# Kernel optimization log

Measured on AMD Instinct MI355X. Metric: run time of the kernel, lower is better.

The kernel has to match this reference:

```python
import jax, jax.numpy as jnp
import numpy as np

C, H, W = 64, 282, 282
PILLAR_SIZE = 0.16
RANGE_MIN = -22.0


def _scatter_forward(PFN_input, PFN_output):
    # PFN_input: [B, 2, P, 1] pillar (x, y) coords; PFN_output: [B, C, P] features
    x = PFN_input[:, 0, :, 0]  # [B, P]
    y = PFN_input[:, 1, :, 0]  # [B, P]
    valid = x != 0  # original uses nonzero(PFN_input[b,0,:,0]) as pillar list
    # digitize into grid cells (equivalent of get_grid over arange(-22,22,0.16))
    xg = jnp.floor((x - RANGE_MIN) / PILLAR_SIZE).astype(jnp.int32)
    yg = jnp.floor((y - RANGE_MIN) / PILLAR_SIZE).astype(jnp.int32)
    # route invalid pillars to an out-of-bounds index; jax scatter drops OOB updates
    xg = jnp.where(valid, jnp.clip(xg, 0, W - 1), W)
    yg = jnp.where(valid, jnp.clip(yg, 0, H - 1), H)

    def scatter_one(xgb, ygb, feats):  # xgb,ygb: [P]; feats: [C, P]
        canvas = jnp.zeros((C, H, W), feats.dtype)
        return canvas.at[:, ygb, xgb].set(feats)

    return jax.vmap(scatter_one)(xg, yg, PFN_output)  # [B, C, H, W]


def setup_inputs() -> dict:
    key = jax.random.key(0)
    k1, k2 = jax.random.split(key)
    B, P = 4, 12000
    PFN_input = jax.random.uniform(k1, (B, 2, P, 1), dtype=jnp.float32,
                                   minval=-22.0, maxval=22.0)
    PFN_output = jax.random.normal(k2, (B, C, P), dtype=jnp.float32)
    return {"PFN_input": PFN_input, "PFN_output": PFN_output}


def reference(PFN_input, PFN_output):
    return _scatter_forward(PFN_input, PFN_output)
```

## Files before the change

### kernel.cpp

```cpp
#include <hip/hip_runtime.h>

#define NB 4
#define NC 64
#define NH 282
#define NW 282
#define NP 12000
#define HWC (NH * NW)
#define QHW (HWC / 4)
#define CLAIM_INTS (NB * HWC)
#define SPLIT 8

__device__ __align__(16) int g_claim[CLAIM_INTS];

__global__ void pps_init_kernel() {
    int gid = blockIdx.x * blockDim.x + threadIdx.x;
    if (gid < CLAIM_INTS / 4) {
        ((int4*)g_claim)[gid] = make_int4(-1, -1, -1, -1);
    }
}

__global__ void pps_claim_kernel(const float* __restrict__ pfn_in) {
    int gid = blockIdx.x * blockDim.x + threadIdx.x;
    if (gid >= NB * NP) return;
    int b = gid / NP;
    int p = gid - b * NP;
    const float* base = pfn_in + (size_t)b * 2 * NP;
    float x = base[p];
    if (x == 0.0f) return;
    float y = base[NP + p];
    int xg = (int)floorf((x + 22.0f) * 6.25f);
    int yg = (int)floorf((y + 22.0f) * 6.25f);
    xg = min(max(xg, 0), NW - 1);
    yg = min(max(yg, 0), NH - 1);
    atomicMax(&g_claim[b * HWC + yg * NW + xg], p);
}

__global__ __launch_bounds__(256) void pps_fill2_kernel(
        const float* __restrict__ pfn_out, float4* __restrict__ out) {
    __shared__ float row[NP];
    int wg = blockIdx.x;
    int s = wg & (SPLIT - 1);
    int plane = wg / SPLIT;
    int b = plane >> 6;

    const float4* src4 = (const float4*)(pfn_out + (size_t)plane * NP);
    for (int i = threadIdx.x; i < NP / 4; i += 256) {
        ((float4*)row)[i] = src4[i];
    }
    __syncthreads();

    const int4* cl = (const int4*)(g_claim + (size_t)b * HWC);
    float4* dst = out + (size_t)plane * QHW;
    const int chunk = (QHW + SPLIT - 1) / SPLIT;
    int q0 = s * chunk;
    int q1 = min(q0 + chunk, QHW);
    for (int q = q0 + (int)threadIdx.x; q < q1; q += 256) {
        int4 c4 = cl[q];
        float4 v;
        v.x = (c4.x >= 0) ? row[c4.x] : 0.0f;
        v.y = (c4.y >= 0) ? row[c4.y] : 0.0f;
        v.z = (c4.z >= 0) ? row[c4.z] : 0.0f;
        v.w = (c4.w >= 0) ? row[c4.w] : 0.0f;
        dst[q] = v;
    }
}

extern "C" void kernel_launch(void* const* d_in, const int* in_sizes, int n_in,
                              void* d_out, int out_size, void* d_ws, size_t ws_size,
                              hipStream_t stream) {
    const float* pfn_in  = (const float*)d_in[0];
    const float* pfn_out = (const float*)d_in[1];
    float* out = (float*)d_out;
    (void)d_ws; (void)ws_size;

    {
        int total = CLAIM_INTS / 4;
        int threads = 256;
        pps_init_kernel<<<(total + threads - 1) / threads, threads, 0, stream>>>();
    }
    {
        int total = NB * NP;
        int threads = 256;
        pps_claim_kernel<<<(total + threads - 1) / threads, threads, 0, stream>>>(pfn_in);
    }
    {
        int blocks = NB * NC * SPLIT;
        pps_fill2_kernel<<<blocks, 256, 0, stream>>>(pfn_out, (float4*)out);
    }
}
```

Baseline: 126.6 us.

## Drop LDS staging of feature rows; gather directly from global with unrolled 2D grid

The fill kernel no longer copies each 12000-float feature plane into shared memory before scattering. Each thread now reads its claim indices (batched four at a time) and gathers feature values straight from global memory, relying on the cache. The grid becomes 2D, with many small chunks per plane instead of eight large ones. This removes the per-block 48KB LDS load and the barrier, and raises occupancy. In exchange the gathers become scattered global/L2 reads.

```diff
diff --git a/kernel.cpp b/kernel.cpp
--- a/kernel.cpp
+++ b/kernel.cpp
@@ -8,7 +8,10 @@
 #define HWC (NH * NW)
 #define QHW (HWC / 4)
 #define CLAIM_INTS (NB * HWC)
-#define SPLIT 8
+#define UNROLL 4
+#define FBLK 256
+#define CHUNK (FBLK * UNROLL)
+#define NXBLK ((QHW + CHUNK - 1) / CHUNK)
 
 __device__ __align__(16) int g_claim[CLAIM_INTS];
 
@@ -35,33 +38,33 @@
     atomicMax(&g_claim[b * HWC + yg * NW + xg], p);
 }
 
-__global__ __launch_bounds__(256) void pps_fill2_kernel(
+__global__ __launch_bounds__(FBLK) void pps_fill3_kernel(
         const float* __restrict__ pfn_out, float4* __restrict__ out) {
-    __shared__ float row[NP];
-    int wg = blockIdx.x;
-    int s = wg & (SPLIT - 1);
-    int plane = wg / SPLIT;
-    int b = plane >> 6;
+    const int plane = blockIdx.y;
+    const int b = plane >> 6;
+    const int q0 = blockIdx.x * CHUNK + threadIdx.x;
+    const int4* __restrict__ cl = (const int4*)(g_claim + b * HWC);
+    const float* __restrict__ row = pfn_out + (size_t)plane * NP;
+    float4* __restrict__ dst = out + (size_t)plane * QHW;
 
-    const float4* src4 = (const float4*)(pfn_out + (size_t)plane * NP);
-    for (int i = threadIdx.x; i < NP / 4; i += 256) {
-        ((float4*)row)[i] = src4[i];
+    int4 c[UNROLL];
+    #pragma unroll
+    for (int k = 0; k < UNROLL; ++k) {
+        int q = q0 + k * FBLK;
+        if (q < QHW) c[k] = cl[q];
     }
-    __syncthreads();
-
-    const int4* cl = (const int4*)(g_claim + (size_t)b * HWC);
-    float4* dst = out + (size_t)plane * QHW;
-    const int chunk = (QHW + SPLIT - 1) / SPLIT;
-    int q0 = s * chunk;
-    int q1 = min(q0 + chunk, QHW);
-    for (int q = q0 + (int)threadIdx.x; q < q1; q += 256) {
-        int4 c4 = cl[q];
-        float4 v;
-        v.x = (c4.x >= 0) ? row[c4.x] : 0.0f;
-        v.y = (c4.y >= 0) ? row[c4.y] : 0.0f;
-        v.z = (c4.z >= 0) ? row[c4.z] : 0.0f;
-        v.w = (c4.w >= 0) ? row[c4.w] : 0.0f;
-        dst[q] = v;
+    #pragma unroll
+    for (int k = 0; k < UNROLL; ++k) {
+        int q = q0 + k * FBLK;
+        if (q < QHW) {
+            int4 c4 = c[k];
+            float4 v;
+            v.x = (c4.x >= 0) ? row[c4.x] : 0.0f;
+            v.y = (c4.y >= 0) ? row[c4.y] : 0.0f;
+            v.z = (c4.z >= 0) ? row[c4.z] : 0.0f;
+            v.w = (c4.w >= 0) ? row[c4.w] : 0.0f;
+            dst[q] = v;
+        }
     }
 }
 
@@ -70,21 +73,19 @@
                               hipStream_t stream) {
     const float* pfn_in  = (const float*)d_in[0];
     const float* pfn_out = (const float*)d_in[1];
-    float* out = (float*)d_out;
+    float4* out = (float4*)d_out;
     (void)d_ws; (void)ws_size;
 
     {
         int total = CLAIM_INTS / 4;
-        int threads = 256;
-        pps_init_kernel<<<(total + threads - 1) / threads, threads, 0, stream>>>();
+        pps_init_kernel<<<(total + 255) / 256, 256, 0, stream>>>();
     }
     {
         int total = NB * NP;
-        int threads = 256;
-        pps_claim_kernel<<<(total + threads - 1) / threads, threads, 0, stream>>>(pfn_in);
+        pps_claim_kernel<<<(total + 255) / 256, 256, 0, stream>>>(pfn_in);
     }
     {
-        int blocks = NB * NC * SPLIT;
-        pps_fill2_kernel<<<blocks, 256, 0, stream>>>(pfn_out, (float4*)out);
+        dim3 grid(NXBLK, NB * NC);
+        pps_fill3_kernel<<<grid, FBLK, 0, stream>>>(pfn_out, out);
     }
 }
```

Measured after the change: 119.7 us. 1.06x faster.
